# Kernel tuning notes

Hardware: AMD Instinct MI355X
Metric: run time of the kernel (lower is better)

## Reference

```python
import jax, jax.numpy as jnp
import numpy as np

B, S, IN = 32, 512, 19
DE, DD = 256, 128      # encoder / decoder d_model
HE, HD = 8, 4          # heads
LE, LD = 6, 2          # layers
FE, FD = 4 * DE, 4 * DD
EPS = 1e-5


def _ln(x, g, b):
    m = x.mean(-1, keepdims=True)
    v = ((x - m) ** 2).mean(-1, keepdims=True)
    return (x - m) / jnp.sqrt(v + EPS) * g + b


def _mha(x, qkv_w, qkv_b, out_w, out_b, kpad, nh):
    Bq, Sq, D = x.shape
    dh = D // nh
    qkv = x @ qkv_w.T + qkv_b
    q, k, v = jnp.split(qkv, 3, axis=-1)
    hs = lambda t: t.reshape(Bq, Sq, nh, dh).transpose(0, 2, 1, 3)  # -> [B,h,S,dh]
    q, k, v = hs(q), hs(k), hs(v)
    scores = jnp.einsum('bhqd,bhkd->bhqk', q, k) / float(np.sqrt(dh))
    scores = jnp.where(kpad[:, None, None, :], -1e9, scores)  # mask padded keys
    attn = jax.nn.softmax(scores, axis=-1)
    o = jnp.einsum('bhqk,bhkd->bhqd', attn, v).transpose(0, 2, 1, 3).reshape(Bq, Sq, D)
    return o @ out_w.T + out_b


def _block(x, p, kpad, nh):
    qkv_w, qkv_b, ow, ob, f1w, f1b, f2w, f2b, g1, b1, g2, b2 = p
    x = _ln(x + _mha(x, qkv_w, qkv_b, ow, ob, kpad, nh), g1, b1)
    h = jax.nn.relu(x @ f1w.T + f1b) @ f2w.T + f2b
    return _ln(x + h, g2, b2)


def _run(x, ps, kpad, nh, L):
    for i in range(L):
        x = _block(x, tuple(p[i] for p in ps), kpad, nh)
    return x


def _forward(event_tensor, w_in_enc, b_in_enc,
             enc_qkv_w, enc_qkv_b, enc_out_w, enc_out_b,
             enc_f1_w, enc_f1_b, enc_f2_w, enc_f2_b,
             enc_g1, enc_b1, enc_g2, enc_b2,
             mask_token, e2d_w,
             dec_qkv_w, dec_qkv_b, dec_out_w, dec_out_b,
             dec_f1_w, dec_f1_b, dec_f2_w, dec_f2_b,
             dec_g1, dec_b1, dec_g2, dec_b2,
             qh_w, qh_b, dth_w, dth_b,
             attention_mask, pred_mask):
    visible = attention_mask & (~pred_mask)
    counts = visible.sum(axis=1)                                  # [B]
    order = jnp.argsort(~visible, axis=1, stable=True)            # visible positions packed first, in order
    tok = event_tensor @ w_in_enc.T + b_in_enc                    # [B,S,DE]
    vis = jnp.take_along_axis(tok, order[:, :, None], axis=1)
    pos = jnp.arange(S)
    enc_pad = pos[None, :] >= counts[:, None]                      # True = padded slot
    vis = jnp.where(enc_pad[:, :, None], 0.0, vis)
    enc_ps = (enc_qkv_w, enc_qkv_b, enc_out_w, enc_out_b, enc_f1_w, enc_f1_b,
              enc_f2_w, enc_f2_b, enc_g1, enc_b1, enc_g2, enc_b2)
    enc_out = _run(vis, enc_ps, enc_pad, HE, LE)
    dec_vis = enc_out @ e2d_w.T                                    # [B,S,DD]
    idx = jnp.cumsum(visible.astype(jnp.int32), axis=1) - 1        # position -> packed index
    gathered = jnp.take_along_axis(dec_vis, jnp.clip(idx, 0)[:, :, None], axis=1)
    dec_in = jnp.where(visible[:, :, None], gathered, mask_token)  # mask token at masked/pad slots
    dec_ps = (dec_qkv_w, dec_qkv_b, dec_out_w, dec_out_b, dec_f1_w, dec_f1_b,
              dec_f2_w, dec_f2_b, dec_g1, dec_b1, dec_g2, dec_b2)
    dec_out = _run(dec_in, dec_ps, ~attention_mask, HD, LD)
    q = dec_out @ qh_w.T + qh_b
    dt = dec_out @ dth_w.T + dth_b
    return jnp.concatenate([q, dt], axis=-1)                       # [B,S,2]


def setup_inputs():
    key = jax.random.key(0)
    ks = iter(jax.random.split(key, 64))
    nrm = lambda shp, s=0.02: jax.random.normal(next(ks), shp, jnp.float32) * s
    d = {}
    d['event_tensor'] = jax.random.normal(next(ks), (B, S, IN), jnp.float32)
    lengths = jax.random.randint(next(ks), (B,), S // 2, S + 1)
    pos = jnp.arange(S)
    am = pos[None, :] < lengths[:, None]
    pm = (jax.random.uniform(next(ks), (B, S)) < 0.75) & am
    pm = pm.at[:, 0].set(False)  # guarantee >=1 visible token per row
    d['attention_mask'] = am
    d['pred_mask'] = pm
    d['w_in_enc'] = nrm((DE, IN)); d['b_in_enc'] = jnp.zeros((DE,), jnp.float32)
    d['enc_qkv_w'] = nrm((LE, 3 * DE, DE)); d['enc_qkv_b'] = jnp.zeros((LE, 3 * DE), jnp.float32)
    d['enc_out_w'] = nrm((LE, DE, DE));     d['enc_out_b'] = jnp.zeros((LE, DE), jnp.float32)
    d['enc_f1_w'] = nrm((LE, FE, DE));      d['enc_f1_b'] = jnp.zeros((LE, FE), jnp.float32)
    d['enc_f2_w'] = nrm((LE, DE, FE));      d['enc_f2_b'] = jnp.zeros((LE, DE), jnp.float32)
    d['enc_g1'] = jnp.ones((LE, DE), jnp.float32); d['enc_b1'] = jnp.zeros((LE, DE), jnp.float32)
    d['enc_g2'] = jnp.ones((LE, DE), jnp.float32); d['enc_b2'] = jnp.zeros((LE, DE), jnp.float32)
    d['mask_token'] = nrm((DD,))
    d['e2d_w'] = nrm((DD, DE))
    d['dec_qkv_w'] = nrm((LD, 3 * DD, DD)); d['dec_qkv_b'] = jnp.zeros((LD, 3 * DD), jnp.float32)
    d['dec_out_w'] = nrm((LD, DD, DD));     d['dec_out_b'] = jnp.zeros((LD, DD), jnp.float32)
    d['dec_f1_w'] = nrm((LD, FD, DD));      d['dec_f1_b'] = jnp.zeros((LD, FD), jnp.float32)
    d['dec_f2_w'] = nrm((LD, DD, FD));      d['dec_f2_b'] = jnp.zeros((LD, DD), jnp.float32)
    d['dec_g1'] = jnp.ones((LD, DD), jnp.float32); d['dec_b1'] = jnp.zeros((LD, DD), jnp.float32)
    d['dec_g2'] = jnp.ones((LD, DD), jnp.float32); d['dec_b2'] = jnp.zeros((LD, DD), jnp.float32)
    d['qh_w'] = nrm((1, DD));  d['qh_b'] = jnp.zeros((1,), jnp.float32)
    d['dth_w'] = nrm((1, DD)); d['dth_b'] = jnp.zeros((1,), jnp.float32)
    return d


def reference(event_tensor, attention_mask, pred_mask, w_in_enc, b_in_enc,
              enc_qkv_w, enc_qkv_b, enc_out_w, enc_out_b,
              enc_f1_w, enc_f1_b, enc_f2_w, enc_f2_b,
              enc_g1, enc_b1, enc_g2, enc_b2,
              mask_token, e2d_w,
              dec_qkv_w, dec_qkv_b, dec_out_w, dec_out_b,
              dec_f1_w, dec_f1_b, dec_f2_w, dec_f2_b,
              dec_g1, dec_b1, dec_g2, dec_b2,
              qh_w, qh_b, dth_w, dth_b):
    return _forward(event_tensor, w_in_enc, b_in_enc,
                    enc_qkv_w, enc_qkv_b, enc_out_w, enc_out_b,
                    enc_f1_w, enc_f1_b, enc_f2_w, enc_f2_b,
                    enc_g1, enc_b1, enc_g2, enc_b2,
                    mask_token, e2d_w,
                    dec_qkv_w, dec_qkv_b, dec_out_w, dec_out_b,
                    dec_f1_w, dec_f1_b, dec_f2_w, dec_f2_b,
                    dec_g1, dec_b1, dec_g2, dec_b2,
                    qh_w, qh_b, dth_w, dth_b,
                    attention_mask, pred_mask)
```

## Files before the change

### kernel.cpp

```cpp
#include <hip/hip_runtime.h>
#include <hip/hip_bf16.h>

#define B_ 32
#define S_ 512
#define IN_ 19
#define DE_ 256
#define DD_ 128
#define HE_ 8
#define HD_ 4
#define LE_ 6
#define LD_ 2
#define FE_ 1024
#define FD_ 512
#define DH_ 32

typedef __attribute__((ext_vector_type(8))) short short8;
typedef __attribute__((ext_vector_type(4))) float f32x4;

__device__ __forceinline__ short f2bf(float f) {
    union { float f; unsigned u; } x; x.f = f;
    unsigned r = x.u + 0x7fff + ((x.u >> 16) & 1);
    return (short)(r >> 16);
}
__device__ __forceinline__ float bf2f(short s) {
    union { unsigned u; float f; } x; x.u = ((unsigned)(unsigned short)s) << 16;
    return x.f;
}

#define GLL16(g, l) __builtin_amdgcn_global_load_lds( \
    (const __attribute__((address_space(1))) void*)(g), \
    (__attribute__((address_space(3))) void*)(l), 16, 0, 0)

#define QSCALE 0.2550653169f

#define NCONV 9
struct ConvTab {
    const float* src[NCONV];
    short* dst[NCONV];
    int len[NCONV];
};
__global__ __launch_bounds__(256) void conv_kernel(ConvTab tab, int total) {
    int i = blockIdx.x * 256 + threadIdx.x;
    if (i >= total) return;
    int j = i;
    for (int e = 0; e < NCONV; ++e) {
        if (j < tab.len[e]) { tab.dst[e][j] = f2bf(tab.src[e][j]); return; }
        j -= tab.len[e];
    }
}

__global__ __launch_bounds__(S_) void plan_kernel(
    const int* __restrict__ am, const int* __restrict__ pm,
    int* __restrict__ counts, int* __restrict__ lengths, int* __restrict__ order,
    int* __restrict__ visible, int* __restrict__ idx) {
    int b = blockIdx.x, s = threadIdx.x;
    __shared__ int sc[S_];
    int a = (am[b * S_ + s] != 0);
    int v = a && (pm[b * S_ + s] == 0);
    visible[b * S_ + s] = v;
    sc[s] = v | (a << 16);
    __syncthreads();
#pragma unroll
    for (int off = 1; off < S_; off <<= 1) {
        int t = (s >= off) ? sc[s - off] : 0;
        __syncthreads();
        sc[s] += t;
        __syncthreads();
    }
    int incl = sc[s] & 0xffff;
    int tot = sc[S_ - 1];
    int total = tot & 0xffff;
    if (s == 0) { counts[b] = total; lengths[b] = tot >> 16; }
    idx[b * S_ + s] = (incl > 0) ? incl - 1 : 0;
    if (v) order[b * S_ + incl - 1] = s;
    else   order[b * S_ + total + (s - incl)] = s;
}

__global__ __launch_bounds__(DE_) void enc_embed_kernel(
    const float* __restrict__ ev, const float* __restrict__ w, const float* __restrict__ bias,
    const int* __restrict__ counts, const int* __restrict__ order, short* __restrict__ out) {
    int bs = blockIdx.x;
    int b = bs / S_, s = bs % S_;
    int d = threadIdx.x;
    __shared__ float e[IN_];
    bool padded = (s >= counts[b]);
    int src = order[bs];
    if (threadIdx.x < IN_)
        e[threadIdx.x] = padded ? 0.f : ev[(size_t)(b * S_ + src) * IN_ + threadIdx.x];
    __syncthreads();
    float acc = bias[d];
#pragma unroll
    for (int i = 0; i < IN_; ++i) acc += e[i] * w[d * IN_ + i];
    out[(size_t)bs * DE_ + d] = padded ? f2bf(0.f) : f2bf(acc);
}

template <bool RELU, bool QKV>
__global__ __launch_bounds__(256) void gemm_mfma(
    const short* __restrict__ A, const short* __restrict__ Wt, const float* __restrict__ bias,
    short* __restrict__ C, int M, int N, int K,
    short* __restrict__ qb, short* __restrict__ kb, short* __restrict__ vtb, int H, int D,
    const int* __restrict__ live) {
    int bm = blockIdx.y * 64, bn = blockIdx.x * 64;
    if (live && (bm & (S_ - 1)) >= live[bm >> 9]) return;
    __shared__ short As[64][32];
    __shared__ short Bs[64][32];
    int t = threadIdx.x;
    int wave = t >> 6, lane = t & 63;
    int wm = (wave >> 1) * 32, wn = (wave & 1) * 32;
    int c = lane & 15, quad = lane >> 4;
    f32x4 acc[2][2];
#pragma unroll
    for (int i = 0; i < 2; ++i)
#pragma unroll
        for (int j = 0; j < 2; ++j) acc[i][j] = (f32x4){0.f, 0.f, 0.f, 0.f};

    const short* gA = A + (size_t)(bm + wave * 16 + (lane >> 2)) * K + (lane & 3) * 8;
    const short* gB = Wt + (size_t)(bn + wave * 16 + (lane >> 2)) * K + (lane & 3) * 8;

    for (int k0 = 0; k0 < K; k0 += 32) {
        GLL16(gA + k0, &As[wave * 16][0]);
        GLL16(gB + k0, &Bs[wave * 16][0]);
        __syncthreads();
        short8 a0 = *(const short8*)&As[wm + c][quad * 8];
        short8 a1 = *(const short8*)&As[wm + 16 + c][quad * 8];
        short8 b0 = *(const short8*)&Bs[wn + c][quad * 8];
        short8 b1 = *(const short8*)&Bs[wn + 16 + c][quad * 8];
        acc[0][0] = __builtin_amdgcn_mfma_f32_16x16x32_bf16(a0, b0, acc[0][0], 0, 0, 0);
        acc[0][1] = __builtin_amdgcn_mfma_f32_16x16x32_bf16(a0, b1, acc[0][1], 0, 0, 0);
        acc[1][0] = __builtin_amdgcn_mfma_f32_16x16x32_bf16(a1, b0, acc[1][0], 0, 0, 0);
        acc[1][1] = __builtin_amdgcn_mfma_f32_16x16x32_bf16(a1, b1, acc[1][1], 0, 0, 0);
        __syncthreads();
    }
#pragma unroll
    for (int mt = 0; mt < 2; ++mt)
#pragma unroll
        for (int nt = 0; nt < 2; ++nt)
#pragma unroll
            for (int r = 0; r < 4; ++r) {
                int R = bm + wm + mt * 16 + quad * 4 + r;
                int Ncol = bn + wn + nt * 16 + c;
                float v = acc[mt][nt][r] + (bias ? bias[Ncol] : 0.f);
                if (RELU) v = fmaxf(v, 0.f);
                if (!QKV) {
                    C[(size_t)R * N + Ncol] = f2bf(v);
                } else {
                    int s = R & (S_ - 1), b2 = R >> 9;
                    if (Ncol < D) {
                        int h = Ncol >> 5, d = Ncol & 31;
                        qb[(((size_t)b2 * H + h) * S_ + s) * DH_ + d] = f2bf(v * QSCALE);
                    } else if (Ncol < 2 * D) {
                        int n2 = Ncol - D, h = n2 >> 5, d = n2 & 31;
                        kb[(((size_t)b2 * H + h) * S_ + s) * DH_ + d] = f2bf(v);
                    } else {
                        int n2 = Ncol - 2 * D, h = n2 >> 5, d = n2 & 31;
                        vtb[(((size_t)b2 * H + h) * DH_ + d) * S_ + s] = f2bf(v);
                    }
                }
            }
}

__global__ __launch_bounds__(256) void attn_flash(
    const short* __restrict__ qb, const short* __restrict__ kb, const short* __restrict__ vtb,
    const int* __restrict__ limit_arr, const int* __restrict__ qlim,
    short* __restrict__ o, int H, int D) {
    int b = blockIdx.z, h = blockIdx.y;
    if (qlim && (int)(blockIdx.x * 64) >= qlim[b]) return;
    int wave = threadIdx.x >> 6, lane = threadIdx.x & 63;
    int q0 = blockIdx.x * 64 + wave * 16;
    int c = lane & 15, quad = lane >> 4;
    size_t bh = (size_t)b * H + h;
    __shared__ short PtAll[4][16][132];
    short (*Pt)[132] = PtAll[wave];

    f32x4 zero = (f32x4){0.f, 0.f, 0.f, 0.f};
    short8 aq = *(const short8*)&qb[(bh * S_ + q0 + c) * DH_ + quad * 8];
    const short* kbase = kb + bh * S_ * DH_;
    const short* vbase = vtb + bh * DH_ * S_;

    int limit = limit_arr[b];
    int nchunks = (limit + 127) >> 7;

    float lrow[4] = {0.f, 0.f, 0.f, 0.f};
    f32x4 o0 = zero, o1 = zero;

    for (int kc = 0; kc < nchunks; ++kc) {
        f32x4 s[8];
#pragma unroll
        for (int nt = 0; nt < 8; ++nt) {
            short8 bk = *(const short8*)&kbase[(size_t)(kc * 128 + nt * 16 + c) * DH_ + quad * 8];
            s[nt] = __builtin_amdgcn_mfma_f32_16x16x32_bf16(aq, bk, zero, 0, 0, 0);
        }
#pragma unroll
        for (int nt = 0; nt < 8; ++nt) {
            bool ok = (kc * 128 + nt * 16 + c) < limit;
#pragma unroll
            for (int r = 0; r < 4; ++r) {
                float p = ok ? exp2f(s[nt][r]) : 0.f;
                s[nt][r] = p;
                lrow[r] += p;
            }
        }
#pragma unroll
        for (int nt = 0; nt < 8; ++nt)
#pragma unroll
            for (int r = 0; r < 4; ++r)
                Pt[quad * 4 + r][nt * 16 + c] = f2bf(s[nt][r]);
#pragma unroll
        for (int kk = 0; kk < 4; ++kk) {
            short8 ap = *(const short8*)&Pt[c][kk * 32 + quad * 8];
            short8 b0 = *(const short8*)&vbase[(size_t)c * S_ + kc * 128 + kk * 32 + quad * 8];
            short8 b1 = *(const short8*)&vbase[(size_t)(16 + c) * S_ + kc * 128 + kk * 32 + quad * 8];
            o0 = __builtin_amdgcn_mfma_f32_16x16x32_bf16(ap, b0, o0, 0, 0, 0);
            o1 = __builtin_amdgcn_mfma_f32_16x16x32_bf16(ap, b1, o1, 0, 0, 0);
        }
    }
#pragma unroll
    for (int r = 0; r < 4; ++r) {
        float l = lrow[r];
        l += __shfl_xor(l, 1);
        l += __shfl_xor(l, 2);
        l += __shfl_xor(l, 4);
        l += __shfl_xor(l, 8);
        float inv = 1.f / l;
        int row = quad * 4 + r;
        size_t base = (size_t)(b * S_ + q0 + row) * D + h * DH_;
        o[base + c] = f2bf(o0[r] * inv);
        o[base + 16 + c] = f2bf(o1[r] * inv);
    }
}

template <int D>
__global__ __launch_bounds__(64) void add_ln_kernel(
    const short* __restrict__ x, const short* __restrict__ h,
    const float* __restrict__ g, const float* __restrict__ be,
    short* __restrict__ out, const int* __restrict__ live) {
    constexpr int E = D / 64;
    int row = blockIdx.x, t = threadIdx.x;
    if (live && (row & (S_ - 1)) >= live[row >> 9]) return;
    const short* px = x + (size_t)row * D + t * E;
    const short* ph = h + (size_t)row * D + t * E;
    float v[E];
    float s = 0.f;
#pragma unroll
    for (int e = 0; e < E; ++e) {
        v[e] = bf2f(px[e]) + bf2f(ph[e]);
        s += v[e];
    }
#pragma unroll
    for (int off = 32; off; off >>= 1) s += __shfl_xor(s, off, 64);
    float m = s / D;
    float s2 = 0.f;
#pragma unroll
    for (int e = 0; e < E; ++e) {
        float d = v[e] - m;
        s2 += d * d;
    }
#pragma unroll
    for (int off = 32; off; off >>= 1) s2 += __shfl_xor(s2, off, 64);
    float rstd = rsqrtf(s2 / D + 1e-5f);
    short* po = out + (size_t)row * D + t * E;
#pragma unroll
    for (int e = 0; e < E; ++e)
        po[e] = f2bf((v[e] - m) * rstd * g[t * E + e] + be[t * E + e]);
}

__global__ __launch_bounds__(DD_) void dec_embed_kernel(
    const short* __restrict__ dec_vis, const float* __restrict__ mask_token,
    const int* __restrict__ visible, const int* __restrict__ idx, short* __restrict__ out) {
    int bs = blockIdx.x, d = threadIdx.x;
    int b = bs / S_;
    short val = visible[bs] ? dec_vis[(size_t)(b * S_ + idx[bs]) * DD_ + d]
                            : f2bf(mask_token[d]);
    out[(size_t)bs * DD_ + d] = val;
}

__global__ __launch_bounds__(64) void head_kernel(
    const short* __restrict__ x, const float* __restrict__ qw, const float* __restrict__ qb,
    const float* __restrict__ dw, const float* __restrict__ db, float* __restrict__ out) {
    int row = blockIdx.x, t = threadIdx.x;
    float v0 = bf2f(x[(size_t)row * DD_ + t]);
    float v1 = bf2f(x[(size_t)row * DD_ + 64 + t]);
    float q = v0 * qw[t] + v1 * qw[64 + t];
    float dt = v0 * dw[t] + v1 * dw[64 + t];
#pragma unroll
    for (int off = 32; off; off >>= 1) {
        q += __shfl_xor(q, off, 64);
        dt += __shfl_xor(dt, off, 64);
    }
    if (t == 0) {
        out[(size_t)row * 2 + 0] = q + qb[0];
        out[(size_t)row * 2 + 1] = dt + db[0];
    }
}

extern "C" void kernel_launch(void* const* d_in, const int* in_sizes, int n_in,
                              void* d_out, int out_size, void* d_ws, size_t ws_size,
                              hipStream_t stream) {
    const float* ev      = (const float*)d_in[0];
    const int*  am       = (const int*)d_in[1];
    const int*  pm       = (const int*)d_in[2];
    const float* w_in    = (const float*)d_in[3];
    const float* b_in    = (const float*)d_in[4];
    const float* eqkv_w  = (const float*)d_in[5];
    const float* eqkv_b  = (const float*)d_in[6];
    const float* eout_w  = (const float*)d_in[7];
    const float* eout_b  = (const float*)d_in[8];
    const float* ef1_w   = (const float*)d_in[9];
    const float* ef1_b   = (const float*)d_in[10];
    const float* ef2_w   = (const float*)d_in[11];
    const float* ef2_b   = (const float*)d_in[12];
    const float* eg1     = (const float*)d_in[13];
    const float* eb1     = (const float*)d_in[14];
    const float* eg2     = (const float*)d_in[15];
    const float* eb2     = (const float*)d_in[16];
    const float* mask_tok= (const float*)d_in[17];
    const float* e2d_w   = (const float*)d_in[18];
    const float* dqkv_w  = (const float*)d_in[19];
    const float* dqkv_b  = (const float*)d_in[20];
    const float* dout_w  = (const float*)d_in[21];
    const float* dout_b  = (const float*)d_in[22];
    const float* df1_w   = (const float*)d_in[23];
    const float* df1_b   = (const float*)d_in[24];
    const float* df2_w   = (const float*)d_in[25];
    const float* df2_b   = (const float*)d_in[26];
    const float* dg1     = (const float*)d_in[27];
    const float* db1     = (const float*)d_in[28];
    const float* dg2     = (const float*)d_in[29];
    const float* db2     = (const float*)d_in[30];
    const float* qh_w    = (const float*)d_in[31];
    const float* qh_b    = (const float*)d_in[32];
    const float* dth_w   = (const float*)d_in[33];
    const float* dth_b   = (const float*)d_in[34];
    float* out = (float*)d_out;

    const int BS = B_ * S_;
    char* ws = (char*)d_ws;
    int* counts  = (int*)ws;
    int* lengths = counts + 32;
    int* order   = lengths + 32;
    int* visible = order + BS;
    int* idx     = visible + BS;

    short* wb = (short*)(ws + 256 * 1024);
    const int L_eqkv = LE_ * 3 * DE_ * DE_;
    const int L_eout = LE_ * DE_ * DE_;
    const int L_ef1  = LE_ * FE_ * DE_;
    const int L_ef2  = LE_ * DE_ * FE_;
    const int L_e2d  = DD_ * DE_;
    const int L_dqkv = LD_ * 3 * DD_ * DD_;
    const int L_dout = LD_ * DD_ * DD_;
    const int L_df1  = LD_ * FD_ * DD_;
    const int L_df2  = LD_ * DD_ * FD_;
    short* w_eqkv = wb;
    short* w_eout = w_eqkv + L_eqkv;
    short* w_ef1  = w_eout + L_eout;
    short* w_ef2  = w_ef1 + L_ef1;
    short* w_e2d  = w_ef2 + L_ef2;
    short* w_dqkv = w_e2d + L_e2d;
    short* w_dout = w_dqkv + L_dqkv;
    short* w_df1  = w_dout + L_dout;
    short* w_df2  = w_df1 + L_df1;
    const int convTotal = L_eqkv + L_eout + L_ef1 + L_ef2 + L_e2d + L_dqkv + L_dout + L_df1 + L_df2;

    short* bx    = (short*)(ws + 12 * 1024 * 1024);
    short* qbuf  = bx   + (size_t)BS * DE_;
    short* kbuf  = qbuf + (size_t)B_ * HE_ * S_ * DH_;
    short* vtbuf = kbuf + (size_t)B_ * HE_ * S_ * DH_;
    short* battn = vtbuf + (size_t)B_ * HE_ * S_ * DH_;
    short* bt    = battn + (size_t)BS * DE_;
    short* hid   = bt + (size_t)BS * DE_;

    ConvTab tab;
    tab.src[0] = eqkv_w; tab.dst[0] = w_eqkv; tab.len[0] = L_eqkv;
    tab.src[1] = eout_w; tab.dst[1] = w_eout; tab.len[1] = L_eout;
    tab.src[2] = ef1_w;  tab.dst[2] = w_ef1;  tab.len[2] = L_ef1;
    tab.src[3] = ef2_w;  tab.dst[3] = w_ef2;  tab.len[3] = L_ef2;
    tab.src[4] = e2d_w;  tab.dst[4] = w_e2d;  tab.len[4] = L_e2d;
    tab.src[5] = dqkv_w; tab.dst[5] = w_dqkv; tab.len[5] = L_dqkv;
    tab.src[6] = dout_w; tab.dst[6] = w_dout; tab.len[6] = L_dout;
    tab.src[7] = df1_w;  tab.dst[7] = w_df1;  tab.len[7] = L_df1;
    tab.src[8] = df2_w;  tab.dst[8] = w_df2;  tab.len[8] = L_df2;
    conv_kernel<<<(convTotal + 255) / 256, 256, 0, stream>>>(tab, convTotal);

    plan_kernel<<<B_, S_, 0, stream>>>(am, pm, counts, lengths, order, visible, idx);
    enc_embed_kernel<<<BS, DE_, 0, stream>>>(ev, w_in, b_in, counts, order, bx);

    for (int l = 0; l < LE_; ++l) {
        gemm_mfma<false, true><<<dim3(3 * DE_ / 64, BS / 64), 256, 0, stream>>>(
            bx, w_eqkv + (size_t)l * 3 * DE_ * DE_, eqkv_b + (size_t)l * 3 * DE_,
            nullptr, BS, 3 * DE_, DE_, qbuf, kbuf, vtbuf, HE_, DE_, counts);
        attn_flash<<<dim3(S_ / 64, HE_, B_), 256, 0, stream>>>(
            qbuf, kbuf, vtbuf, counts, counts, battn, HE_, DE_);
        gemm_mfma<false, false><<<dim3(DE_ / 64, BS / 64), 256, 0, stream>>>(
            battn, w_eout + (size_t)l * DE_ * DE_, eout_b + (size_t)l * DE_,
            bt, BS, DE_, DE_, nullptr, nullptr, nullptr, 0, 0, counts);
        add_ln_kernel<DE_><<<BS, 64, 0, stream>>>(
            bx, bt, eg1 + (size_t)l * DE_, eb1 + (size_t)l * DE_, bx, counts);
        gemm_mfma<true, false><<<dim3(FE_ / 64, BS / 64), 256, 0, stream>>>(
            bx, w_ef1 + (size_t)l * FE_ * DE_, ef1_b + (size_t)l * FE_,
            hid, BS, FE_, DE_, nullptr, nullptr, nullptr, 0, 0, counts);
        gemm_mfma<false, false><<<dim3(DE_ / 64, BS / 64), 256, 0, stream>>>(
            hid, w_ef2 + (size_t)l * DE_ * FE_, ef2_b + (size_t)l * DE_,
            bt, BS, DE_, FE_, nullptr, nullptr, nullptr, 0, 0, counts);
        add_ln_kernel<DE_><<<BS, 64, 0, stream>>>(
            bx, bt, eg2 + (size_t)l * DE_, eb2 + (size_t)l * DE_, bx, counts);
    }

    gemm_mfma<false, false><<<dim3(DD_ / 64, BS / 64), 256, 0, stream>>>(
        bx, w_e2d, nullptr, bt, BS, DD_, DE_, nullptr, nullptr, nullptr, 0, 0, counts);
    dec_embed_kernel<<<BS, DD_, 0, stream>>>(bt, mask_tok, visible, idx, bx);

    for (int l = 0; l < LD_; ++l) {
        gemm_mfma<false, true><<<dim3(3 * DD_ / 64, BS / 64), 256, 0, stream>>>(
            bx, w_dqkv + (size_t)l * 3 * DD_ * DD_, dqkv_b + (size_t)l * 3 * DD_, nullptr,
            BS, 3 * DD_, DD_, qbuf, kbuf, vtbuf, HD_, DD_, nullptr);
        attn_flash<<<dim3(S_ / 64, HD_, B_), 256, 0, stream>>>(
            qbuf, kbuf, vtbuf, lengths, nullptr, battn, HD_, DD_);
        gemm_mfma<false, false><<<dim3(DD_ / 64, BS / 64), 256, 0, stream>>>(
            battn, w_dout + (size_t)l * DD_ * DD_, dout_b + (size_t)l * DD_,
            bt, BS, DD_, DD_, nullptr, nullptr, nullptr, 0, 0, nullptr);
        add_ln_kernel<DD_><<<BS, 64, 0, stream>>>(
            bx, bt, dg1 + (size_t)l * DD_, db1 + (size_t)l * DD_, bx, nullptr);
        gemm_mfma<true, false><<<dim3(FD_ / 64, BS / 64), 256, 0, stream>>>(
            bx, w_df1 + (size_t)l * FD_ * DD_, df1_b + (size_t)l * FD_,
            hid, BS, FD_, DD_, nullptr, nullptr, nullptr, 0, 0, nullptr);
        gemm_mfma<false, false><<<dim3(DD_ / 64, BS / 64), 256, 0, stream>>>(
            hid, w_df2 + (size_t)l * DD_ * FD_, df2_b + (size_t)l * DD_,
            bt, BS, DD_, FD_, nullptr, nullptr, nullptr, 0, 0, nullptr);
        add_ln_kernel<DD_><<<BS, 64, 0, stream>>>(
            bx, bt, dg2 + (size_t)l * DD_, db2 + (size_t)l * DD_, bx, nullptr);
    }

    head_kernel<<<BS, 64, 0, stream>>>(bx, qh_w, qh_b, dth_w, dth_b, out);
}
```

Measured before the change: 877.3 us.

## Fuse residual-add and LayerNorm into GEMM epilogues and prologues via row stats

Removes the separate add+LayerNorm kernels. The out-projection and FFN2 GEMMs now add the residual in their epilogue, store the un-normalized sum and accumulate per-row sum and sum-of-squares with atomics. The next consumer GEMM or the head applies the normalization when it loads its A operand. This saves kernel launches and a full activation read/write pass per LayerNorm. In exchange, the LN-prologue GEMMs lose the async global-to-LDS load for A and redo the normalization in every N-tile block. The one-pass variance is less numerically stable, and the stats buffers must be zeroed (folded into conv_kernel).

```diff
diff --git a/kernel.cpp b/kernel.cpp
--- a/kernel.cpp
+++ b/kernel.cpp
@@ -13,6 +13,7 @@
 #define FE_ 1024
 #define FD_ 512
 #define DH_ 32
+#define BS_ (B_ * S_)
 
 typedef __attribute__((ext_vector_type(8))) short short8;
 typedef __attribute__((ext_vector_type(4))) float f32x4;
@@ -32,6 +33,11 @@
     (__attribute__((address_space(3))) void*)(l), 16, 0, 0)
 
 #define QSCALE 0.2550653169f
+
+#define WB_OFF    262144
+#define STATS_OFF 10551296
+#define ACT_OFF   12648448
+#define STATS_FLOATS (16 * BS_ * 2)
 
 #define NCONV 9
 struct ConvTab {
@@ -39,13 +45,16 @@
     short* dst[NCONV];
     int len[NCONV];
 };
-__global__ __launch_bounds__(256) void conv_kernel(ConvTab tab, int total) {
+__global__ __launch_bounds__(256) void conv_kernel(ConvTab tab, int total, float* statsBase) {
     int i = blockIdx.x * 256 + threadIdx.x;
-    if (i >= total) return;
-    int j = i;
-    for (int e = 0; e < NCONV; ++e) {
-        if (j < tab.len[e]) { tab.dst[e][j] = f2bf(tab.src[e][j]); return; }
-        j -= tab.len[e];
+    if (i < total) {
+        int j = i;
+        for (int e = 0; e < NCONV; ++e) {
+            if (j < tab.len[e]) { tab.dst[e][j] = f2bf(tab.src[e][j]); return; }
+            j -= tab.len[e];
+        }
+    } else if (i < total + STATS_FLOATS) {
+        statsBase[i - total] = 0.f;
     }
 }
 
@@ -94,12 +103,15 @@
     out[(size_t)bs * DE_ + d] = padded ? f2bf(0.f) : f2bf(acc);
 }
 
-template <bool RELU, bool QKV>
+template <bool RELU, bool QKV, bool LNA, bool RESOUT>
 __global__ __launch_bounds__(256) void gemm_mfma(
     const short* __restrict__ A, const short* __restrict__ Wt, const float* __restrict__ bias,
     short* __restrict__ C, int M, int N, int K,
     short* __restrict__ qb, short* __restrict__ kb, short* __restrict__ vtb, int H, int D,
-    const int* __restrict__ live) {
+    const int* __restrict__ live,
+    const float* __restrict__ statsA, const float* __restrict__ gA, const float* __restrict__ beA,
+    const float* __restrict__ statsR, const float* __restrict__ gR, const float* __restrict__ beR,
+    float* __restrict__ statsOut) {
     int bm = blockIdx.y * 64, bn = blockIdx.x * 64;
     if (live && (bm & (S_ - 1)) >= live[bm >> 9]) return;
     __shared__ short As[64][32];
@@ -114,12 +126,32 @@
 #pragma unroll
         for (int j = 0; j < 2; ++j) acc[i][j] = (f32x4){0.f, 0.f, 0.f, 0.f};
 
-    const short* gA = A + (size_t)(bm + wave * 16 + (lane >> 2)) * K + (lane & 3) * 8;
-    const short* gB = Wt + (size_t)(bn + wave * 16 + (lane >> 2)) * K + (lane & 3) * 8;
+    int srow = lane >> 2, scol = (lane & 3) * 8;
+    const short* gAp = A + (size_t)(bm + wave * 16 + srow) * K + scol;
+    const short* gBp = Wt + (size_t)(bn + wave * 16 + srow) * K + scol;
+
+    float mA = 0.f, rA = 0.f;
+    if (LNA) {
+        int grow = bm + wave * 16 + srow;
+        float s = statsA[grow * 2], sq = statsA[grow * 2 + 1];
+        mA = s / K;
+        rA = rsqrtf(sq / K - mA * mA + 1e-5f);
+    }
 
     for (int k0 = 0; k0 < K; k0 += 32) {
-        GLL16(gA + k0, &As[wave * 16][0]);
-        GLL16(gB + k0, &Bs[wave * 16][0]);
+        if (LNA) {
+            short8 raw = *(const short8*)(gAp + k0);
+            const float* gc = gA + k0 + scol;
+            const float* bc = beA + k0 + scol;
+            short8 ov;
+#pragma unroll
+            for (int j = 0; j < 8; ++j)
+                ov[j] = f2bf((bf2f(raw[j]) - mA) * rA * gc[j] + bc[j]);
+            *(short8*)&As[wave * 16 + srow][scol] = ov;
+        } else {
+            GLL16(gAp + k0, &As[wave * 16][0]);
+        }
+        GLL16(gBp + k0, &Bs[wave * 16][0]);
         __syncthreads();
         short8 a0 = *(const short8*)&As[wm + c][quad * 8];
         short8 a1 = *(const short8*)&As[wm + 16 + c][quad * 8];
@@ -134,16 +166,21 @@
 #pragma unroll
     for (int mt = 0; mt < 2; ++mt)
 #pragma unroll
-        for (int nt = 0; nt < 2; ++nt)
-#pragma unroll
-            for (int r = 0; r < 4; ++r) {
-                int R = bm + wm + mt * 16 + quad * 4 + r;
+        for (int r = 0; r < 4; ++r) {
+            int R = bm + wm + mt * 16 + quad * 4 + r;
+            float mR = 0.f, rR = 0.f;
+            if (RESOUT && statsR) {
+                float s = statsR[R * 2], sq = statsR[R * 2 + 1];
+                mR = s / N;
+                rR = rsqrtf(sq / N - mR * mR + 1e-5f);
+            }
+            float rowsum = 0.f, rowsq = 0.f;
+#pragma unroll
+            for (int nt = 0; nt < 2; ++nt) {
                 int Ncol = bn + wn + nt * 16 + c;
                 float v = acc[mt][nt][r] + (bias ? bias[Ncol] : 0.f);
                 if (RELU) v = fmaxf(v, 0.f);
-                if (!QKV) {
-                    C[(size_t)R * N + Ncol] = f2bf(v);
-                } else {
+                if (QKV) {
                     int s = R & (S_ - 1), b2 = R >> 9;
                     if (Ncol < D) {
                         int h = Ncol >> 5, d = Ncol & 31;
@@ -155,8 +192,31 @@
                         int n2 = Ncol - 2 * D, h = n2 >> 5, d = n2 & 31;
                         vtb[(((size_t)b2 * H + h) * DH_ + d) * S_ + s] = f2bf(v);
                     }
+                } else if (RESOUT) {
+                    short old = C[(size_t)R * N + Ncol];
+                    float res = statsR ? (bf2f(old) - mR) * rR * gR[Ncol] + beR[Ncol]
+                                       : bf2f(old);
+                    float xv = v + res;
+                    short xb = f2bf(xv);
+                    C[(size_t)R * N + Ncol] = xb;
+                    float xr = bf2f(xb);
+                    rowsum += xr;
+                    rowsq += xr * xr;
+                } else {
+                    C[(size_t)R * N + Ncol] = f2bf(v);
                 }
             }
+            if (RESOUT) {
+                rowsum += __shfl_xor(rowsum, 1); rowsq += __shfl_xor(rowsq, 1);
+                rowsum += __shfl_xor(rowsum, 2); rowsq += __shfl_xor(rowsq, 2);
+                rowsum += __shfl_xor(rowsum, 4); rowsq += __shfl_xor(rowsq, 4);
+                rowsum += __shfl_xor(rowsum, 8); rowsq += __shfl_xor(rowsq, 8);
+                if (c == 0) {
+                    atomicAdd(&statsOut[R * 2], rowsum);
+                    atomicAdd(&statsOut[R * 2 + 1], rowsq);
+                }
+            }
+        }
 }
 
 __global__ __launch_bounds__(256) void attn_flash(
@@ -229,41 +289,6 @@
     }
 }
 
-template <int D>
-__global__ __launch_bounds__(64) void add_ln_kernel(
-    const short* __restrict__ x, const short* __restrict__ h,
-    const float* __restrict__ g, const float* __restrict__ be,
-    short* __restrict__ out, const int* __restrict__ live) {
-    constexpr int E = D / 64;
-    int row = blockIdx.x, t = threadIdx.x;
-    if (live && (row & (S_ - 1)) >= live[row >> 9]) return;
-    const short* px = x + (size_t)row * D + t * E;
-    const short* ph = h + (size_t)row * D + t * E;
-    float v[E];
-    float s = 0.f;
-#pragma unroll
-    for (int e = 0; e < E; ++e) {
-        v[e] = bf2f(px[e]) + bf2f(ph[e]);
-        s += v[e];
-    }
-#pragma unroll
-    for (int off = 32; off; off >>= 1) s += __shfl_xor(s, off, 64);
-    float m = s / D;
-    float s2 = 0.f;
-#pragma unroll
-    for (int e = 0; e < E; ++e) {
-        float d = v[e] - m;
-        s2 += d * d;
-    }
-#pragma unroll
-    for (int off = 32; off; off >>= 1) s2 += __shfl_xor(s2, off, 64);
-    float rstd = rsqrtf(s2 / D + 1e-5f);
-    short* po = out + (size_t)row * D + t * E;
-#pragma unroll
-    for (int e = 0; e < E; ++e)
-        po[e] = f2bf((v[e] - m) * rstd * g[t * E + e] + be[t * E + e]);
-}
-
 __global__ __launch_bounds__(DD_) void dec_embed_kernel(
     const short* __restrict__ dec_vis, const float* __restrict__ mask_token,
     const int* __restrict__ visible, const int* __restrict__ idx, short* __restrict__ out) {
@@ -275,11 +300,16 @@
 }
 
 __global__ __launch_bounds__(64) void head_kernel(
-    const short* __restrict__ x, const float* __restrict__ qw, const float* __restrict__ qb,
+    const short* __restrict__ x, const float* __restrict__ stats,
+    const float* __restrict__ g, const float* __restrict__ be,
+    const float* __restrict__ qw, const float* __restrict__ qb,
     const float* __restrict__ dw, const float* __restrict__ db, float* __restrict__ out) {
     int row = blockIdx.x, t = threadIdx.x;
-    float v0 = bf2f(x[(size_t)row * DD_ + t]);
-    float v1 = bf2f(x[(size_t)row * DD_ + 64 + t]);
+    float s = stats[row * 2], sq = stats[row * 2 + 1];
+    float m = s / DD_;
+    float r = rsqrtf(sq / DD_ - m * m + 1e-5f);
+    float v0 = (bf2f(x[(size_t)row * DD_ + t]) - m) * r * g[t] + be[t];
+    float v1 = (bf2f(x[(size_t)row * DD_ + 64 + t]) - m) * r * g[64 + t] + be[64 + t];
     float q = v0 * qw[t] + v1 * qw[64 + t];
     float dt = v0 * dw[t] + v1 * dw[64 + t];
 #pragma unroll
@@ -333,15 +363,14 @@
     const float* dth_b   = (const float*)d_in[34];
     float* out = (float*)d_out;
 
-    const int BS = B_ * S_;
     char* ws = (char*)d_ws;
     int* counts  = (int*)ws;
     int* lengths = counts + 32;
     int* order   = lengths + 32;
-    int* visible = order + BS;
-    int* idx     = visible + BS;
-
-    short* wb = (short*)(ws + 256 * 1024);
+    int* visible = order + BS_;
+    int* idx     = visible + BS_;
+
+    short* wb = (short*)(ws + WB_OFF);
     const int L_eqkv = LE_ * 3 * DE_ * DE_;
     const int L_eout = LE_ * DE_ * DE_;
     const int L_ef1  = LE_ * FE_ * DE_;
@@ -362,13 +391,18 @@
     short* w_df2  = w_df1 + L_df1;
     const int convTotal = L_eqkv + L_eout + L_ef1 + L_ef2 + L_e2d + L_dqkv + L_dout + L_df1 + L_df2;
 
-    short* bx    = (short*)(ws + 12 * 1024 * 1024);
-    short* qbuf  = bx   + (size_t)BS * DE_;
+    float* stats = (float*)(ws + STATS_OFF);
+    float* s1e[LE_], *s2e[LE_], *s1d[LD_], *s2d[LD_];
+    for (int l = 0; l < LE_; ++l) { s1e[l] = stats + (size_t)l * BS_ * 2; s2e[l] = stats + (size_t)(6 + l) * BS_ * 2; }
+    for (int l = 0; l < LD_; ++l) { s1d[l] = stats + (size_t)(12 + l) * BS_ * 2; s2d[l] = stats + (size_t)(14 + l) * BS_ * 2; }
+
+    short* bx    = (short*)(ws + ACT_OFF);
+    short* qbuf  = bx   + (size_t)BS_ * DE_;
     short* kbuf  = qbuf + (size_t)B_ * HE_ * S_ * DH_;
     short* vtbuf = kbuf + (size_t)B_ * HE_ * S_ * DH_;
     short* battn = vtbuf + (size_t)B_ * HE_ * S_ * DH_;
-    short* bt    = battn + (size_t)BS * DE_;
-    short* hid   = bt + (size_t)BS * DE_;
+    short* bt    = battn + (size_t)BS_ * DE_;
+    short* hid   = bt + (size_t)BS_ * DE_;
 
     ConvTab tab;
     tab.src[0] = eqkv_w; tab.dst[0] = w_eqkv; tab.len[0] = L_eqkv;
@@ -380,56 +414,78 @@
     tab.src[6] = dout_w; tab.dst[6] = w_dout; tab.len[6] = L_dout;
     tab.src[7] = df1_w;  tab.dst[7] = w_df1;  tab.len[7] = L_df1;
     tab.src[8] = df2_w;  tab.dst[8] = w_df2;  tab.len[8] = L_df2;
-    conv_kernel<<<(convTotal + 255) / 256, 256, 0, stream>>>(tab, convTotal);
+    conv_kernel<<<(convTotal + STATS_FLOATS + 255) / 256, 256, 0, stream>>>(tab, convTotal, stats);
 
     plan_kernel<<<B_, S_, 0, stream>>>(am, pm, counts, lengths, order, visible, idx);
-    enc_embed_kernel<<<BS, DE_, 0, stream>>>(ev, w_in, b_in, counts, order, bx);
+    enc_embed_kernel<<<BS_, DE_, 0, stream>>>(ev, w_in, b_in, counts, order, bx);
 
     for (int l = 0; l < LE_; ++l) {
-        gemm_mfma<false, true><<<dim3(3 * DE_ / 64, BS / 64), 256, 0, stream>>>(
-            bx, w_eqkv + (size_t)l * 3 * DE_ * DE_, eqkv_b + (size_t)l * 3 * DE_,
-            nullptr, BS, 3 * DE_, DE_, qbuf, kbuf, vtbuf, HE_, DE_, counts);
+        const float* pstats = (l > 0) ? s2e[l - 1] : nullptr;
+        const float* pg = eg2 + (size_t)(l ? l - 1 : 0) * DE_;
+        const float* pb = eb2 + (size_t)(l ? l - 1 : 0) * DE_;
+        if (l == 0)
+            gemm_mfma<false, true, false, false><<<dim3(3 * DE_ / 64, BS_ / 64), 256, 0, stream>>>(
+                bx, w_eqkv + (size_t)l * 3 * DE_ * DE_, eqkv_b + (size_t)l * 3 * DE_,
+                nullptr, BS_, 3 * DE_, DE_, qbuf, kbuf, vtbuf, HE_, DE_, counts,
+                nullptr, nullptr, nullptr, nullptr, nullptr, nullptr, nullptr);
+        else
+            gemm_mfma<false, true, true, false><<<dim3(3 * DE_ / 64, BS_ / 64), 256, 0, stream>>>(
+                bx, w_eqkv + (size_t)l * 3 * DE_ * DE_, eqkv_b + (size_t)l * 3 * DE_,
+                nullptr, BS_, 3 * DE_, DE_, qbuf, kbuf, vtbuf, HE_, DE_, counts,
+                pstats, pg, pb, nullptr, nullptr, nullptr, nullptr);
         attn_flash<<<dim3(S_ / 64, HE_, B_), 256, 0, stream>>>(
             qbuf, kbuf, vtbuf, counts, counts, battn, HE_, DE_);
-        gemm_mfma<false, false><<<dim3(DE_ / 64, BS / 64), 256, 0, stream>>>(
+        gemm_mfma<false, false, false, true><<<dim3(DE_ / 64, BS_ / 64), 256, 0, stream>>>(
             battn, w_eout + (size_t)l * DE_ * DE_, eout_b + (size_t)l * DE_,
-            bt, BS, DE_, DE_, nullptr, nullptr, nullptr, 0, 0, counts);
-        add_ln_kernel<DE_><<<BS, 64, 0, stream>>>(
-            bx, bt, eg1 + (size_t)l * DE_, eb1 + (size_t)l * DE_, bx, counts);
-        gemm_mfma<true, false><<<dim3(FE_ / 64, BS / 64), 256, 0, stream>>>(
+            bx, BS_, DE_, DE_, nullptr, nullptr, nullptr, 0, 0, counts,
+            nullptr, nullptr, nullptr, pstats, pg, pb, s1e[l]);
+        gemm_mfma<true, false, true, false><<<dim3(FE_ / 64, BS_ / 64), 256, 0, stream>>>(
             bx, w_ef1 + (size_t)l * FE_ * DE_, ef1_b + (size_t)l * FE_,
-            hid, BS, FE_, DE_, nullptr, nullptr, nullptr, 0, 0, counts);
-        gemm_mfma<false, false><<<dim3(DE_ / 64, BS / 64), 256, 0, stream>>>(
+            hid, BS_, FE_, DE_, nullptr, nullptr, nullptr, 0, 0, counts,
+            s1e[l], eg1 + (size_t)l * DE_, eb1 + (size_t)l * DE_, nullptr, nullptr, nullptr, nullptr);
+        gemm_mfma<false, false, false, true><<<dim3(DE_ / 64, BS_ / 64), 256, 0, stream>>>(
             hid, w_ef2 + (size_t)l * DE_ * FE_, ef2_b + (size_t)l * DE_,
-            bt, BS, DE_, FE_, nullptr, nullptr, nullptr, 0, 0, counts);
-        add_ln_kernel<DE_><<<BS, 64, 0, stream>>>(
-            bx, bt, eg2 + (size_t)l * DE_, eb2 + (size_t)l * DE_, bx, counts);
-    }
-
-    gemm_mfma<false, false><<<dim3(DD_ / 64, BS / 64), 256, 0, stream>>>(
-        bx, w_e2d, nullptr, bt, BS, DD_, DE_, nullptr, nullptr, nullptr, 0, 0, counts);
-    dec_embed_kernel<<<BS, DD_, 0, stream>>>(bt, mask_tok, visible, idx, bx);
+            bx, BS_, DE_, FE_, nullptr, nullptr, nullptr, 0, 0, counts,
+            nullptr, nullptr, nullptr, s1e[l], eg1 + (size_t)l * DE_, eb1 + (size_t)l * DE_, s2e[l]);
+    }
+
+    gemm_mfma<false, false, true, false><<<dim3(DD_ / 64, BS_ / 64), 256, 0, stream>>>(
+        bx, w_e2d, nullptr, bt, BS_, DD_, DE_, nullptr, nullptr, nullptr, 0, 0, counts,
+        s2e[LE_ - 1], eg2 + (size_t)(LE_ - 1) * DE_, eb2 + (size_t)(LE_ - 1) * DE_,
+        nullptr, nullptr, nullptr, nullptr);
+    dec_embed_kernel<<<BS_, DD_, 0, stream>>>(bt, mask_tok, visible, idx, bx);
 
     for (int l = 0; l < LD_; ++l) {
-        gemm_mfma<false, true><<<dim3(3 * DD_ / 64, BS / 64), 256, 0, stream>>>(
-            bx, w_dqkv + (size_t)l * 3 * DD_ * DD_, dqkv_b + (size_t)l * 3 * DD_, nullptr,
-            BS, 3 * DD_, DD_, qbuf, kbuf, vtbuf, HD_, DD_, nullptr);
+        const float* pstats = (l > 0) ? s2d[l - 1] : nullptr;
+        const float* pg = dg2 + (size_t)(l ? l - 1 : 0) * DD_;
+        const float* pb = db2 + (size_t)(l ? l - 1 : 0) * DD_;
+        if (l == 0)
+            gemm_mfma<false, true, false, false><<<dim3(3 * DD_ / 64, BS_ / 64), 256, 0, stream>>>(
+                bx, w_dqkv + (size_t)l * 3 * DD_ * DD_, dqkv_b + (size_t)l * 3 * DD_,
+                nullptr, BS_, 3 * DD_, DD_, qbuf, kbuf, vtbuf, HD_, DD_, nullptr,
+                nullptr, nullptr, nullptr, nullptr, nullptr, nullptr, nullptr);
+        else
+            gemm_mfma<false, true, true, false><<<dim3(3 * DD_ / 64, BS_ / 64), 256, 0, stream>>>(
+                bx, w_dqkv + (size_t)l * 3 * DD_ * DD_, dqkv_b + (size_t)l * 3 * DD_,
+                nullptr, BS_, 3 * DD_, DD_, qbuf, kbuf, vtbuf, HD_, DD_, nullptr,
+                pstats, pg, pb, nullptr, nullptr, nullptr, nullptr);
         attn_flash<<<dim3(S_ / 64, HD_, B_), 256, 0, stream>>>(
             qbuf, kbuf, vtbuf, lengths, nullptr, battn, HD_, DD_);
-        gemm_mfma<false, false><<<dim3(DD_ / 64, BS / 64), 256, 0, stream>>>(
+        gemm_mfma<false, false, false, true><<<dim3(DD_ / 64, BS_ / 64), 256, 0, stream>>>(
             battn, w_dout + (size_t)l * DD_ * DD_, dout_b + (size_t)l * DD_,
-            bt, BS, DD_, DD_, nullptr, nullptr, nullptr, 0, 0, nullptr);
-        add_ln_kernel<DD_><<<BS, 64, 0, stream>>>(
-            bx, bt, dg1 + (size_t)l * DD_, db1 + (size_t)l * DD_, bx, nullptr);
-        gemm_mfma<true, false><<<dim3(FD_ / 64, BS / 64), 256, 0, stream>>>(
+            bx, BS_, DD_, DD_, nullptr, nullptr, nullptr, 0, 0, nullptr,
+            nullptr, nullptr, nullptr, pstats, pg, pb, s1d[l]);
+        gemm_mfma<true, false, true, false><<<dim3(FD_ / 64, BS_ / 64), 256, 0, stream>>>(
             bx, w_df1 + (size_t)l * FD_ * DD_, df1_b + (size_t)l * FD_,
-            hid, BS, FD_, DD_, nullptr, nullptr, nullptr, 0, 0, nullptr);
-        gemm_mfma<false, false><<<dim3(DD_ / 64, BS / 64), 256, 0, stream>>>(
+            hid, BS_, FD_, DD_, nullptr, nullptr, nullptr, 0, 0, nullptr,
+            s1d[l], dg1 + (size_t)l * DD_, db1 + (size_t)l * DD_, nullptr, nullptr, nullptr, nullptr);
+        gemm_mfma<false, false, false, true><<<dim3(DD_ / 64, BS_ / 64), 256, 0, stream>>>(
             hid, w_df2 + (size_t)l * DD_ * FD_, df2_b + (size_t)l * DD_,
-            bt, BS, DD_, FD_, nullptr, nullptr, nullptr, 0, 0, nullptr);
-        add_ln_kernel<DD_><<<BS, 64, 0, stream>>>(
-            bx, bt, dg2 + (size_t)l * DD_, db2 + (size_t)l * DD_, bx, nullptr);
-    }
-
-    head_kernel<<<BS, 64, 0, stream>>>(bx, qh_w, qh_b, dth_w, dth_b, out);
-}
+            bx, BS_, DD_, FD_, nullptr, nullptr, nullptr, 0, 0, nullptr,
+            nullptr, nullptr, nullptr, s1d[l], dg1 + (size_t)l * DD_, db1 + (size_t)l * DD_, s2d[l]);
+    }
+
+    head_kernel<<<BS_, 64, 0, stream>>>(
+        bx, s2d[LD_ - 1], dg2 + (size_t)(LD_ - 1) * DD_, db2 + (size_t)(LD_ - 1) * DD_,
+        qh_w, qh_b, dth_w, dth_b, out);
+}
```

Result: slower. 1.064 ms (+21.3%).
